# Performance work log

Hardware: AMD Instinct MI355X
Metric: run time of the kernel (lower is better)

## Reference

```python
import jax, jax.numpy as jnp
import numpy as np

D_MODEL = 1024
N_HEADS = 16
ADAPTIVE_TEMP = 1.0
LN_EPS = 1e-5


def _sinusoidal_pe(max_len, d_model):
    pos = np.arange(max_len)[:, None].astype(np.float32)
    div = np.exp(np.arange(0, d_model, 2).astype(np.float32) * (-np.log(10000.0) / d_model))
    pe = np.zeros((max_len, d_model), dtype=np.float32)
    pe[:, 0::2] = np.sin(pos * div)
    pe[:, 1::2] = np.cos(pos * div)
    return jnp.asarray(pe)


def _mlp2(q, w1, b1, w2, b2):
    # Linear(1,h) -> ReLU -> Linear(h,d)
    return jax.nn.relu(q @ w1 + b1) @ w2 + b2


def setup_inputs() -> dict:
    key = jax.random.key(0)
    ks = jax.random.split(key, 24)
    B, T, D = 2, 2048, D_MODEL
    H2 = D // 2
    s = 0.02
    inp = {
        "x": jax.random.normal(ks[0], (B, T, D), jnp.float32),
        "quantile": jax.random.uniform(ks[1], (B, 1), jnp.float32),
        "quantile_importance": jax.random.uniform(ks[2], (100,), jnp.float32),
        "Wq": jax.random.normal(ks[3], (D, D), jnp.float32) * s,
        "bq": jnp.zeros((D,), jnp.float32),
        "Wk": jax.random.normal(ks[4], (D, D), jnp.float32) * s,
        "bk": jnp.zeros((D,), jnp.float32),
        "Wv": jax.random.normal(ks[5], (D, D), jnp.float32) * s,
        "bv": jnp.zeros((D,), jnp.float32),
        "Wo": jax.random.normal(ks[6], (D, D), jnp.float32) * s,
        "bo": jnp.zeros((D,), jnp.float32),
        "qpq_w1": jax.random.normal(ks[7], (1, H2), jnp.float32) * s,
        "qpq_b1": jnp.zeros((H2,), jnp.float32),
        "qpq_w2": jax.random.normal(ks[8], (H2, D), jnp.float32) * s,
        "qpq_b2": jnp.zeros((D,), jnp.float32),
        "qpk_w1": jax.random.normal(ks[9], (1, H2), jnp.float32) * s,
        "qpk_b1": jnp.zeros((H2,), jnp.float32),
        "qpk_w2": jax.random.normal(ks[10], (H2, D), jnp.float32) * s,
        "qpk_b2": jnp.zeros((D,), jnp.float32),
        "qpv_w1": jax.random.normal(ks[11], (1, H2), jnp.float32) * s,
        "qpv_b1": jnp.zeros((H2,), jnp.float32),
        "qpv_w2": jax.random.normal(ks[12], (H2, D), jnp.float32) * s,
        "qpv_b2": jnp.zeros((D,), jnp.float32),
        "ln_g": jnp.ones((D,), jnp.float32),
        "ln_b": jnp.zeros((D,), jnp.float32),
    }
    return inp


def reference(x, quantile, quantile_importance,
              Wq, bq, Wk, bk, Wv, bv, Wo, bo,
              qpq_w1, qpq_b1, qpq_w2, qpq_b2,
              qpk_w1, qpk_b1, qpk_w2, qpk_b2,
              qpv_w1, qpv_b1, qpv_w2, qpv_b2,
              ln_g, ln_b):
    B, T, D = x.shape
    H = N_HEADS
    dk = D // H

    # positional encoding
    x = x + _sinusoidal_pe(T, D)

    # quantile-conditioned embeddings [B, D]
    q_embed = _mlp2(quantile, qpq_w1, qpq_b1, qpq_w2, qpq_b2)
    k_embed = _mlp2(quantile, qpk_w1, qpk_b1, qpk_w2, qpk_b2)
    v_embed = _mlp2(quantile, qpv_w1, qpv_b1, qpv_w2, qpv_b2)

    # importance weight per batch (no-grad buffer lookup)
    buf = jax.lax.stop_gradient(quantile_importance)
    idx = jnp.clip((quantile[:, 0] * 100).astype(jnp.int32), 0, 99)
    mx = buf.max()
    imp = buf[idx]
    imp = jnp.where(mx > 0, imp / mx, imp)  # [B]

    Q = (x @ Wq + bq) + q_embed[:, None, :]
    K = (x @ Wk + bk) + k_embed[:, None, :]
    V = (x @ Wv + bv) + v_embed[:, None, :]

    # [B, H, T, dk]
    Q = Q.reshape(B, T, H, dk).transpose(0, 2, 1, 3)
    K = K.reshape(B, T, H, dk).transpose(0, 2, 1, 3)
    V = V.reshape(B, T, H, dk).transpose(0, 2, 1, 3)

    scores = jnp.einsum('bhtd,bhsd->bhts', Q, K) / jnp.sqrt(jnp.float32(dk))
    scale = 1.0 + imp * ADAPTIVE_TEMP  # [B]
    scores = scores * scale[:, None, None, None]

    attn = jax.nn.softmax(scores, axis=-1)  # dropout is identity at inference
    out = jnp.einsum('bhts,bhsd->bhtd', attn, V)
    out = out.transpose(0, 2, 1, 3).reshape(B, T, D)
    out = out @ Wo + bo

    y = x + out
    mu = y.mean(axis=-1, keepdims=True)
    var = y.var(axis=-1, keepdims=True)
    return (y - mu) / jnp.sqrt(var + LN_EPS) * ln_g + ln_b
```

## Files before the change

kernel.cpp:

```cpp
#include <hip/hip_runtime.h>

#define D 1024
#define T 2048
#define BATCH 2
#define NR 4096
#define NH 16
#define HID 512

typedef unsigned short u16;
typedef unsigned int u32;
typedef unsigned long long u64;
typedef float f32x4 __attribute__((ext_vector_type(4)));
typedef float f32x16 __attribute__((ext_vector_type(16)));
typedef __bf16 bf16x8 __attribute__((ext_vector_type(8)));

__device__ __forceinline__ u16 f2bf(float f) {
    union { __bf16 h; u16 u; } c; c.h = (__bf16)f; return c.u;
}

__device__ __forceinline__ u32 cvtpk(float a, float b) {
    u32 r;
    asm("v_cvt_pk_bf16_f32 %0, %1, %2" : "=v"(r) : "v"(a), "v"(b));
    return r;
}

__device__ __forceinline__ void plswap(u32& x, u32& y) {
    asm volatile("v_permlane32_swap_b32 %0, %1" : "+v"(x), "+v"(y));
}

__device__ __forceinline__ float fmax3(float a, float b, float c) {
    float r; asm("v_max3_f32 %0, %1, %2, %3" : "=v"(r) : "v"(a), "v"(b), "v"(c)); return r;
}

__device__ __forceinline__ float vmax16(const f32x16& v) {
    float c0 = fmax3(v[0], v[1], v[2]);
    float c1 = fmax3(v[3], v[4], v[5]);
    float c2 = fmax3(v[6], v[7], v[8]);
    float c3 = fmax3(v[9], v[10], v[11]);
    c0 = fmax3(c0, v[12], v[13]);
    c1 = fmax3(c1, v[14], v[15]);
    c0 = fmax3(c0, c1, c2);
    return fmaxf(c0, c3);
}

__device__ __forceinline__ void gload16(const u16* g, u16* l) {
    __builtin_amdgcn_global_load_lds(
        (const __attribute__((address_space(1))) unsigned int*)g,
        (__attribute__((address_space(3))) unsigned int*)l,
        16, 0, 0);
}

__device__ __forceinline__ int swz8(int row) {
    return (row & 7) ^ ((row >> 3) & 3);
}

__global__ __launch_bounds__(256) void k_mlp1(const float* __restrict__ qtl,
        const float* __restrict__ w1q, const float* __restrict__ b1q, const float* __restrict__ w2q,
        const float* __restrict__ w1k, const float* __restrict__ b1k, const float* __restrict__ w2k,
        const float* __restrict__ w1v, const float* __restrict__ b1v, const float* __restrict__ w2v,
        const float* __restrict__ qimp, float* __restrict__ part, float* __restrict__ scl)
{
    int dc = blockIdx.x;
    int jc = blockIdx.y;
    int wb = blockIdx.z;
    int which = wb >> 1, b = wb & 1;
    const float *w1, *b1, *w2;
    if (which == 0)      { w1 = w1q; b1 = b1q; w2 = w2q; }
    else if (which == 1) { w1 = w1k; b1 = b1k; w2 = w2k; }
    else                 { w1 = w1v; b1 = b1v; w2 = w2v; }
    int tid = threadIdx.x;
    __shared__ float h[128];
    if (tid < 128) {
        int j = jc * 128 + tid;
        h[tid] = fmaxf(qtl[b] * w1[j] + b1[j], 0.0f);
    }
    __syncthreads();
    int d = dc * 256 + tid;
    float acc = 0.0f;
    for (int j = 0; j < 128; ++j) acc += h[j] * w2[(size_t)(jc * 128 + j) * D + d];
    part[((size_t)wb * 4 + jc) * D + d] = acc;
    if (dc == 0 && jc == 0 && wb == 0 && tid < BATCH) {
        float mx = qimp[0];
        for (int i = 1; i < 100; ++i) mx = fmaxf(mx, qimp[i]);
        float q = qtl[tid];
        int idx = (int)(q * 100.0f);
        idx = idx < 0 ? 0 : (idx > 99 ? 99 : idx);
        float imp = qimp[idx];
        if (mx > 0.0f) imp /= mx;
        scl[tid] = 1.0f + imp;
    }
}

__global__ __launch_bounds__(256) void k_mlp2(const float* __restrict__ part,
        const float* __restrict__ b2q, const float* __restrict__ b2k, const float* __restrict__ b2v,
        float* __restrict__ embeds)
{
    int dc = blockIdx.x;
    int wb = blockIdx.y;
    int which = wb >> 1;
    const float* b2 = which == 0 ? b2q : which == 1 ? b2k : b2v;
    int d = dc * 256 + threadIdx.x;
    float acc = b2[d];
    #pragma unroll
    for (int jc = 0; jc < 4; ++jc) acc += part[((size_t)wb * 4 + jc) * D + d];
    embeds[(size_t)wb * D + d] = acc;
}

__global__ __launch_bounds__(256) void k_pe(const float* __restrict__ x,
                                            float* __restrict__ xpe, u16* __restrict__ xpeb)
{
    int idx = (blockIdx.x * 256 + threadIdx.x) * 4;
    int d = idx & (D - 1);
    int t = (idx >> 10) & (T - 1);
    const float KL = -0.0089944731946f;
    float ft = (float)t;
    float dv0 = __expf((float)d * KL);
    float dv1 = __expf((float)(d + 2) * KL);
    float a0 = ft * dv0, a1 = ft * dv1;
    float4 xv = *reinterpret_cast<const float4*>(x + idx);
    float4 r;
    r.x = xv.x + __sinf(a0);
    r.y = xv.y + __cosf(a0);
    r.z = xv.z + __sinf(a1);
    r.w = xv.w + __cosf(a1);
    *reinterpret_cast<float4*>(xpe + idx) = r;
    ushort4 o;
    o.x = f2bf(r.x); o.y = f2bf(r.y); o.z = f2bf(r.z); o.w = f2bf(r.w);
    *reinterpret_cast<ushort4*>(xpeb + idx) = o;
}

__global__ __launch_bounds__(256) void k_wconv(const float* __restrict__ Wq, const float* __restrict__ Wk,
                                               const float* __restrict__ Wv, const float* __restrict__ Wo,
                                               u16* __restrict__ Wt)
{
    __shared__ float tile[64][65];
    int z = blockIdx.z;
    const float* W = z == 0 ? Wq : z == 1 ? Wk : z == 2 ? Wv : Wo;
    u16* out = Wt + (size_t)z * D * D;
    int n0 = blockIdx.x * 64, k0 = blockIdx.y * 64;
    int r = threadIdx.x >> 4;
    int c4 = (threadIdx.x & 15) * 4;
    #pragma unroll
    for (int rr = 0; rr < 64; rr += 16) {
        float4 v = *reinterpret_cast<const float4*>(W + (size_t)(k0 + r + rr) * D + n0 + c4);
        tile[r + rr][c4 + 0] = v.x; tile[r + rr][c4 + 1] = v.y;
        tile[r + rr][c4 + 2] = v.z; tile[r + rr][c4 + 3] = v.w;
    }
    __syncthreads();
    #pragma unroll
    for (int rr = 0; rr < 64; rr += 16) {
        ushort4 o;
        o.x = f2bf(tile[c4 + 0][r + rr]);
        o.y = f2bf(tile[c4 + 1][r + rr]);
        o.z = f2bf(tile[c4 + 2][r + rr]);
        o.w = f2bf(tile[c4 + 3][r + rr]);
        *reinterpret_cast<ushort4*>(out + (size_t)(n0 + r + rr) * D + k0 + c4) = o;
    }
}

__device__ __forceinline__ void gemm128(const u16* __restrict__ Ag, const u16* __restrict__ Bg,
                                        int m0, int n0, f32x4 acc[4][4])
{
    __shared__ u16 As[128 * 64];
    __shared__ u16 Bs[128 * 64];
    const int tid = threadIdx.x;
    const int lane = tid & 63, wave = tid >> 6;
    const int wr = wave >> 1, wc = wave & 1;
    #pragma unroll
    for (int i = 0; i < 4; ++i)
        #pragma unroll
        for (int j = 0; j < 4; ++j)
            #pragma unroll
            for (int e = 0; e < 4; ++e) acc[i][j][e] = 0.0f;

    for (int kt = 0; kt < 16; ++kt) {
        __syncthreads();
        #pragma unroll
        for (int c = 0; c < 4; ++c) {
            int ci = c * 256 + tid;
            int row = ci >> 3;
            int sl = (ci & 7) ^ (row & 7);
            gload16(Ag + (size_t)(m0 + row) * D + kt * 64 + sl * 8, As + (size_t)ci * 8);
            gload16(Bg + (size_t)(n0 + row) * D + kt * 64 + sl * 8, Bs + (size_t)ci * 8);
        }
        __syncthreads();
        #pragma unroll
        for (int ks = 0; ks < 2; ++ks) {
            bf16x8 af[4], bfr[4];
            #pragma unroll
            for (int i = 0; i < 4; ++i) {
                int ra = wr * 64 + i * 16 + (lane & 15);
                int sa = ((ks * 4 + (lane >> 4)) ^ (ra & 7));
                af[i] = *reinterpret_cast<const bf16x8*>((const char*)As + ra * 128 + sa * 16);
                int rb = wc * 64 + i * 16 + (lane & 15);
                int sb = ((ks * 4 + (lane >> 4)) ^ (rb & 7));
                bfr[i] = *reinterpret_cast<const bf16x8*>((const char*)Bs + rb * 128 + sb * 16);
            }
            #pragma unroll
            for (int i = 0; i < 4; ++i)
                #pragma unroll
                for (int j = 0; j < 4; ++j)
                    acc[i][j] = __builtin_amdgcn_mfma_f32_16x16x32_bf16(af[i], bfr[j], acc[i][j], 0, 0, 0);
        }
    }
}

__global__ __launch_bounds__(256, 2)
void k_qkv(const u16* __restrict__ A, const u16* __restrict__ Wt,
           const float* __restrict__ bq, const float* __restrict__ bk, const float* __restrict__ bv,
           const float* __restrict__ embeds, const float* __restrict__ scl,
           u16* __restrict__ Qo, u16* __restrict__ Ko, u16* __restrict__ Vt)
{
    int which = blockIdx.z;
    const u16* Bg = Wt + (size_t)which * D * D;
    const float* bias = which == 0 ? bq : which == 1 ? bk : bv;
    const float* emb = embeds + which * (BATCH * D);
    int m0 = blockIdx.x * 128, n0 = blockIdx.y * 128;
    f32x4 acc[4][4];
    gemm128(A, Bg, m0, n0, acc);
    int lane = threadIdx.x & 63, wave = threadIdx.x >> 6;
    int wr = wave >> 1, wc = wave & 1;
    int rowbase = m0 + wr * 64 + ((lane >> 4) << 2);
    int colbase = n0 + wc * 64 + (lane & 15);
    if (which < 2) {
        u16* Out = which == 0 ? Qo : Ko;
        float sc0 = 1.0f, sc1 = 1.0f;
        if (which == 0) {
            sc0 = scl[0] * 0.125f * 1.44269504f;
            sc1 = scl[1] * 0.125f * 1.44269504f;
        }
        #pragma unroll
        for (int j = 0; j < 4; ++j) {
            int c = colbase + j * 16;
            float add0 = bias[c] + emb[c];
            float add1 = bias[c] + emb[D + c];
            #pragma unroll
            for (int i = 0; i < 4; ++i) {
                int rb = rowbase + i * 16;
                #pragma unroll
                for (int jj = 0; jj < 4; ++jj) {
                    int r = rb + jj;
                    float v = (r >> 11) ? (acc[i][j][jj] + add1) * sc1
                                        : (acc[i][j][jj] + add0) * sc0;
                    Out[(size_t)r * D + c] = f2bf(v);
                }
            }
        }
    } else {
        #pragma unroll
        for (int j = 0; j < 4; ++j) {
            int c = colbase + j * 16;
            int hh = c >> 6, cc = c & 63;
            float add0 = bias[c] + emb[c];
            float add1 = bias[c] + emb[D + c];
            #pragma unroll
            for (int i = 0; i < 4; ++i) {
                int rb = rowbase + i * 16;
                int bb = rb >> 11;
                int t = rb & (T - 1);
                float add = bb ? add1 : add0;
                ushort4 o;
                o.x = f2bf(acc[i][j][0] + add);
                o.y = f2bf(acc[i][j][1] + add);
                o.z = f2bf(acc[i][j][2] + add);
                o.w = f2bf(acc[i][j][3] + add);
                *reinterpret_cast<ushort4*>(Vt + ((size_t)((bb * NH + hh) * 64 + cc)) * T + t) = o;
            }
        }
    }
}

__global__ __launch_bounds__(512, 4)
void k_attn(const u16* __restrict__ Q, const u16* __restrict__ K, const u16* __restrict__ Vt,
            u16* __restrict__ AO)
{
    __shared__ u16 Ks[2][2][64 * 64];
    __shared__ u16 Vs[2][2][64 * 64];
    int bh = blockIdx.x;
    int b = bh >> 4, hh = bh & 15;
    int q0 = blockIdx.y * 128;
    int tid = threadIdx.x;
    int lane = tid & 63, w = tid >> 6;
    int half = w >> 2, wq = w & 3;
    int q31 = lane & 31, h = lane >> 5;
    int sh = tid >> 8, sti = tid & 255;
    int kvb = sh * 1024;

    bf16x8 qf[4];
    {
        const u16* qp = Q + (size_t)(b * T + q0 + wq * 32 + q31) * D + hh * 64 + h * 8;
        #pragma unroll
        for (int ds = 0; ds < 4; ++ds)
            qf[ds] = *reinterpret_cast<const bf16x8*>(qp + ds * 16);
    }

    f32x16 o0, o1;
    #pragma unroll
    for (int e = 0; e < 16; ++e) { o0[e] = 0.0f; o1[e] = 0.0f; }
    float m_run = -1e30f, l_run = 0.0f;

    #pragma unroll
    for (int c = 0; c < 2; ++c) {
        int ci = c * 256 + sti;
        int row = ci >> 3;
        int sl = (ci & 7) ^ swz8(row);
        gload16(K + (size_t)(b * T + kvb + row) * D + hh * 64 + sl * 8, Ks[sh][0] + (size_t)ci * 8);
        gload16(Vt + (size_t)(bh * 64 + row) * T + kvb + sl * 8, Vs[sh][0] + (size_t)ci * 8);
    }
    __syncthreads();

    for (int kt = 0; kt < 16; ++kt) {
        int cur = kt & 1;
        if (kt < 15) {
            int t0 = kvb + (kt + 1) * 64;
            #pragma unroll
            for (int c = 0; c < 2; ++c) {
                int ci = c * 256 + sti;
                int row = ci >> 3;
                int sl = (ci & 7) ^ swz8(row);
                gload16(K + (size_t)(b * T + t0 + row) * D + hh * 64 + sl * 8, Ks[sh][cur ^ 1] + (size_t)ci * 8);
                gload16(Vt + (size_t)(bh * 64 + row) * T + t0 + sl * 8, Vs[sh][cur ^ 1] + (size_t)ci * 8);
            }
        }
        const char* Ksc = (const char*)Ks[half][cur];
        const char* Vsc = (const char*)Vs[half][cur];

        f32x16 s[2];
        #pragma unroll
        for (int k2 = 0; k2 < 2; ++k2)
            #pragma unroll
            for (int e = 0; e < 16; ++e) s[k2][e] = 0.0f;
        __builtin_amdgcn_s_setprio(1);
        #pragma unroll
        for (int k2 = 0; k2 < 2; ++k2) {
            int rk = k2 * 32 + q31;
            int xm = swz8(rk);
            #pragma unroll
            for (int ds = 0; ds < 4; ++ds) {
                int sp = (2 * ds + h) ^ xm;
                bf16x8 kf = *reinterpret_cast<const bf16x8*>(Ksc + rk * 128 + sp * 16);
                s[k2] = __builtin_amdgcn_mfma_f32_32x32x16_bf16(kf, qf[ds], s[k2], 0, 0, 0);
            }
        }
        __builtin_amdgcn_s_setprio(0);

        float mt = fmaxf(vmax16(s[0]), vmax16(s[1]));
        mt = fmaxf(mt, __shfl_xor(mt, 32, 64));
        bool skip = __all((int)(mt <= m_run + 11.0f));
        if (!skip) {
            float mn = fmaxf(m_run, mt);
            float corr = __builtin_exp2f(m_run - mn);
            m_run = mn;
            l_run *= corr;
            #pragma unroll
            for (int reg = 0; reg < 16; ++reg) {
                int src = ((reg & 3) + 8 * (reg >> 2)) + ((lane & 32) >> 3);
                float cr = __shfl(corr, src, 64);
                o0[reg] *= cr;
                o1[reg] *= cr;
            }
        }
        float ps0 = 0.0f, ps1 = 0.0f, ps2 = 0.0f, ps3 = 0.0f;
        #pragma unroll
        for (int k2 = 0; k2 < 2; ++k2)
            #pragma unroll
            for (int e = 0; e < 16; ++e) {
                float p = __builtin_exp2f(s[k2][e] - m_run);
                s[k2][e] = p;
                if ((e & 3) == 0) ps0 += p; else if ((e & 3) == 1) ps1 += p;
                else if ((e & 3) == 2) ps2 += p; else ps3 += p;
            }
        float psum = (ps0 + ps1) + (ps2 + ps3);
        psum += __shfl_xor(psum, 32, 64);
        l_run += psum;

        __builtin_amdgcn_s_setprio(1);
        #pragma unroll
        for (int k2 = 0; k2 < 2; ++k2) {
            u32 w0 = cvtpk(s[k2][0], s[k2][1]),   w1 = cvtpk(s[k2][2], s[k2][3]);
            u32 w2 = cvtpk(s[k2][4], s[k2][5]),   w3 = cvtpk(s[k2][6], s[k2][7]);
            u32 w4 = cvtpk(s[k2][8], s[k2][9]),   w5 = cvtpk(s[k2][10], s[k2][11]);
            u32 w6 = cvtpk(s[k2][12], s[k2][13]), w7 = cvtpk(s[k2][14], s[k2][15]);
            plswap(w0, w2); plswap(w1, w3);
            plswap(w4, w6); plswap(w5, w7);
            union { bf16x8 v; u32 u[4]; } plo, phi;
            plo.u[0] = w0; plo.u[1] = w1; plo.u[2] = w2; plo.u[3] = w3;
            phi.u[0] = w4; phi.u[1] = w5; phi.u[2] = w6; phi.u[3] = w7;
            int rv0 = q31, rv1 = 32 + q31;
            int x0 = swz8(rv0), x1 = swz8(rv1);
            int klo = 2 * k2, khi = 2 * k2 + 1;
            bf16x8 vf;
            vf = *reinterpret_cast<const bf16x8*>(Vsc + rv0 * 128 + (((2 * klo + h) ^ x0) << 4));
            o0 = __builtin_amdgcn_mfma_f32_32x32x16_bf16(plo.v, vf, o0, 0, 0, 0);
            vf = *reinterpret_cast<const bf16x8*>(Vsc + rv1 * 128 + (((2 * klo + h) ^ x1) << 4));
            o1 = __builtin_amdgcn_mfma_f32_32x32x16_bf16(plo.v, vf, o1, 0, 0, 0);
            vf = *reinterpret_cast<const bf16x8*>(Vsc + rv0 * 128 + (((2 * khi + h) ^ x0) << 4));
            o0 = __builtin_amdgcn_mfma_f32_32x32x16_bf16(phi.v, vf, o0, 0, 0, 0);
            vf = *reinterpret_cast<const bf16x8*>(Vsc + rv1 * 128 + (((2 * khi + h) ^ x1) << 4));
            o1 = __builtin_amdgcn_mfma_f32_32x32x16_bf16(phi.v, vf, o1, 0, 0, 0);
        }
        __builtin_amdgcn_s_setprio(0);
        __syncthreads();
    }

    float* ML = (float*)Ks;
    float* OB = (float*)Vs;
    if (half == 1) {
        if (h == 0) {
            ML[(wq * 2 + 0) * 32 + q31] = m_run;
            ML[(wq * 2 + 1) * 32 + q31] = l_run;
        }
        #pragma unroll
        for (int reg = 0; reg < 16; ++reg) {
            int row = (reg & 3) + 8 * (reg >> 2) + 4 * h;
            OB[((size_t)wq * 32 + row) * 64 + q31] = o0[reg];
            OB[((size_t)wq * 32 + row) * 64 + 32 + q31] = o1[reg];
        }
    }
    __syncthreads();
    if (half == 0) {
        float mB = ML[(wq * 2 + 0) * 32 + q31];
        float lB = ML[(wq * 2 + 1) * 32 + q31];
        float mn = fmaxf(m_run, mB);
        float ca = __builtin_exp2f(m_run - mn);
        float cb = __builtin_exp2f(mB - mn);
        float lf = ca * l_run + cb * lB;
        float fa = ca / lf, fb = cb / lf;
        #pragma unroll
        for (int reg = 0; reg < 16; ++reg) {
            int src = ((reg & 3) + 8 * (reg >> 2)) + ((lane & 32) >> 3);
            float far = __shfl(fa, src, 64);
            float fbr = __shfl(fb, src, 64);
            int row = (reg & 3) + 8 * (reg >> 2) + 4 * h;
            float b0 = OB[((size_t)wq * 32 + row) * 64 + q31];
            float b1 = OB[((size_t)wq * 32 + row) * 64 + 32 + q31];
            int qr = q0 + wq * 32 + row;
            size_t off = (size_t)(b * T + qr) * D + hh * 64 + q31;
            AO[off] = f2bf(o0[reg] * far + b0 * fbr);
            AO[off + 32] = f2bf(o1[reg] * far + b1 * fbr);
        }
    }
}

__global__ __launch_bounds__(256, 2)
void k_ogemm(const u16* __restrict__ A, const u16* __restrict__ Wt,
             const float* __restrict__ bo, const float* __restrict__ xpe,
             float* __restrict__ y)
{
    int m0 = blockIdx.x * 128, n0 = blockIdx.y * 128;
    f32x4 acc[4][4];
    gemm128(A, Wt, m0, n0, acc);
    int lane = threadIdx.x & 63, wave = threadIdx.x >> 6;
    int wr = wave >> 1, wc = wave & 1;
    int rowbase = m0 + wr * 64 + ((lane >> 4) << 2);
    int colbase = n0 + wc * 64 + (lane & 15);
    #pragma unroll
    for (int j = 0; j < 4; ++j) {
        int c = colbase + j * 16;
        float bc = bo[c];
        #pragma unroll
        for (int i = 0; i < 4; ++i) {
            #pragma unroll
            for (int jj = 0; jj < 4; ++jj) {
                int r = rowbase + i * 16 + jj;
                y[(size_t)r * D + c] = acc[i][j][jj] + bc + xpe[(size_t)r * D + c];
            }
        }
    }
}

__global__ __launch_bounds__(256) void k_ln(const float* __restrict__ y, const float* __restrict__ g,
                                            const float* __restrict__ bb, float* __restrict__ out)
{
    int row = blockIdx.x;
    int tid = threadIdx.x;
    const float* yr = y + (size_t)row * D;
    float4 v = *reinterpret_cast<const float4*>(yr + tid * 4);
    float s = v.x + v.y + v.z + v.w;
    float s2 = v.x * v.x + v.y * v.y + v.z * v.z + v.w * v.w;
    #pragma unroll
    for (int off = 1; off < 64; off <<= 1) {
        s += __shfl_xor(s, off, 64);
        s2 += __shfl_xor(s2, off, 64);
    }
    __shared__ float red[8];
    int wave = tid >> 6, lane = tid & 63;
    if (lane == 0) { red[wave] = s; red[4 + wave] = s2; }
    __syncthreads();
    s = red[0] + red[1] + red[2] + red[3];
    s2 = red[4] + red[5] + red[6] + red[7];
    float mu = s * (1.0f / 1024.0f);
    float var = s2 * (1.0f / 1024.0f) - mu * mu;
    float rstd = rsqrtf(var + 1e-5f);
    float4 gv = *reinterpret_cast<const float4*>(g + tid * 4);
    float4 bv = *reinterpret_cast<const float4*>(bb + tid * 4);
    float4 o;
    o.x = (v.x - mu) * rstd * gv.x + bv.x;
    o.y = (v.y - mu) * rstd * gv.y + bv.y;
    o.z = (v.z - mu) * rstd * gv.z + bv.z;
    o.w = (v.w - mu) * rstd * gv.w + bv.w;
    *reinterpret_cast<float4*>(out + (size_t)row * D + tid * 4) = o;
}

extern "C" void kernel_launch(void* const* d_in, const int* in_sizes, int n_in,
                              void* d_out, int out_size, void* d_ws, size_t ws_size,
                              hipStream_t stream)
{
    const float* x    = (const float*)d_in[0];
    const float* qtl  = (const float*)d_in[1];
    const float* qimp = (const float*)d_in[2];
    const float* Wq = (const float*)d_in[3];
    const float* bq = (const float*)d_in[4];
    const float* Wk = (const float*)d_in[5];
    const float* bk = (const float*)d_in[6];
    const float* Wv = (const float*)d_in[7];
    const float* bv = (const float*)d_in[8];
    const float* Wo = (const float*)d_in[9];
    const float* bo = (const float*)d_in[10];
    const float* qpq_w1 = (const float*)d_in[11];
    const float* qpq_b1 = (const float*)d_in[12];
    const float* qpq_w2 = (const float*)d_in[13];
    const float* qpq_b2 = (const float*)d_in[14];
    const float* qpk_w1 = (const float*)d_in[15];
    const float* qpk_b1 = (const float*)d_in[16];
    const float* qpk_w2 = (const float*)d_in[17];
    const float* qpk_b2 = (const float*)d_in[18];
    const float* qpv_w1 = (const float*)d_in[19];
    const float* qpv_b1 = (const float*)d_in[20];
    const float* qpv_w2 = (const float*)d_in[21];
    const float* qpv_b2 = (const float*)d_in[22];
    const float* ln_g = (const float*)d_in[23];
    const float* ln_b = (const float*)d_in[24];
    (void)in_sizes; (void)n_in; (void)out_size; (void)ws_size;

    char* w = (char*)d_ws;
    float* xpe   = (float*)(w);
    u16* xpeb    = (u16*)(w + (16u << 20));
    u16* Wt      = (u16*)(w + (24u << 20));
    u16* Qb      = (u16*)(w + (32u << 20));
    u16* Kb      = (u16*)(w + (40u << 20));
    u16* Vtb     = (u16*)(w + (48u << 20));
    u16* AOb     = (u16*)(w + (56u << 20));
    float* yb    = (float*)(w + (32u << 20));
    float* emb   = (float*)(w + (64u << 20));
    float* scl   = (float*)(w + (64u << 20) + 32768);
    float* part  = (float*)(w + (64u << 20) + 65536);

    k_mlp1<<<dim3(4, 4, 6), 256, 0, stream>>>(qtl,
        qpq_w1, qpq_b1, qpq_w2,
        qpk_w1, qpk_b1, qpk_w2,
        qpv_w1, qpv_b1, qpv_w2,
        qimp, part, scl);
    k_mlp2<<<dim3(4, 6), 256, 0, stream>>>(part, qpq_b2, qpk_b2, qpv_b2, emb);
    k_pe<<<4096, 256, 0, stream>>>(x, xpe, xpeb);
    k_wconv<<<dim3(16, 16, 4), 256, 0, stream>>>(Wq, Wk, Wv, Wo, Wt);
    k_qkv<<<dim3(32, 8, 3), 256, 0, stream>>>(xpeb, Wt, bq, bk, bv, emb, scl, Qb, Kb, Vtb);
    k_attn<<<dim3(32, 16), 512, 0, stream>>>(Qb, Kb, Vtb, AOb);
    k_ogemm<<<dim3(32, 8), 256, 0, stream>>>(AOb, Wt + (size_t)3 * D * D, bo, xpe, yb);
    k_ln<<<4096, 256, 0, stream>>>(yb, ln_g, ln_b, (float*)d_out);
}
```

Baseline: 159.9 us.

## Load K/V fragments directly from global memory instead of staging in LDS

Removes the double-buffered LDS staging of K and V tiles (global_load_lds plus swizzle) in the attention kernel. Each lane now reads its K and V MFMA fragments straight from global memory, relying on L2/L1 caching, which also removes the per-iteration __syncthreads. This trades LDS traffic and barriers for repeated global loads: the four query waves of a half now each fetch the same K/V data separately, and the loads are no longer software-prefetched one tile ahead.

```diff
diff --git a/kernel.cpp b/kernel.cpp
--- a/kernel.cpp
+++ b/kernel.cpp
@@ -48,10 +48,6 @@
         (const __attribute__((address_space(1))) unsigned int*)g,
         (__attribute__((address_space(3))) unsigned int*)l,
         16, 0, 0);
-}
-
-__device__ __forceinline__ int swz8(int row) {
-    return (row & 7) ^ ((row >> 3) & 3);
 }
 
 __global__ __launch_bounds__(256) void k_mlp1(const float* __restrict__ qtl,
@@ -274,8 +270,8 @@
 void k_attn(const u16* __restrict__ Q, const u16* __restrict__ K, const u16* __restrict__ Vt,
             u16* __restrict__ AO)
 {
-    __shared__ u16 Ks[2][2][64 * 64];
-    __shared__ u16 Vs[2][2][64 * 64];
+    __shared__ float ML[4 * 2 * 32];
+    __shared__ float OB[4 * 32 * 64];
     int bh = blockIdx.x;
     int b = bh >> 4, hh = bh & 15;
     int q0 = blockIdx.y * 128;
@@ -283,8 +279,7 @@
     int lane = tid & 63, w = tid >> 6;
     int half = w >> 2, wq = w & 3;
     int q31 = lane & 31, h = lane >> 5;
-    int sh = tid >> 8, sti = tid & 255;
-    int kvb = sh * 1024;
+    int kvb = half * 1024;
 
     bf16x8 qf[4];
     {
@@ -294,37 +289,17 @@
             qf[ds] = *reinterpret_cast<const bf16x8*>(qp + ds * 16);
     }
 
+    const u16* kp0 = K + (size_t)(b * T + kvb + q31) * D + hh * 64;
+    const u16* kp1 = kp0 + (size_t)32 * D;
+    const u16* vp0 = Vt + (size_t)(bh * 64 + q31) * T + kvb;
+    const u16* vp1 = vp0 + (size_t)32 * T;
+
     f32x16 o0, o1;
     #pragma unroll
     for (int e = 0; e < 16; ++e) { o0[e] = 0.0f; o1[e] = 0.0f; }
     float m_run = -1e30f, l_run = 0.0f;
 
-    #pragma unroll
-    for (int c = 0; c < 2; ++c) {
-        int ci = c * 256 + sti;
-        int row = ci >> 3;
-        int sl = (ci & 7) ^ swz8(row);
-        gload16(K + (size_t)(b * T + kvb + row) * D + hh * 64 + sl * 8, Ks[sh][0] + (size_t)ci * 8);
-        gload16(Vt + (size_t)(bh * 64 + row) * T + kvb + sl * 8, Vs[sh][0] + (size_t)ci * 8);
-    }
-    __syncthreads();
-
     for (int kt = 0; kt < 16; ++kt) {
-        int cur = kt & 1;
-        if (kt < 15) {
-            int t0 = kvb + (kt + 1) * 64;
-            #pragma unroll
-            for (int c = 0; c < 2; ++c) {
-                int ci = c * 256 + sti;
-                int row = ci >> 3;
-                int sl = (ci & 7) ^ swz8(row);
-                gload16(K + (size_t)(b * T + t0 + row) * D + hh * 64 + sl * 8, Ks[sh][cur ^ 1] + (size_t)ci * 8);
-                gload16(Vt + (size_t)(bh * 64 + row) * T + t0 + sl * 8, Vs[sh][cur ^ 1] + (size_t)ci * 8);
-            }
-        }
-        const char* Ksc = (const char*)Ks[half][cur];
-        const char* Vsc = (const char*)Vs[half][cur];
-
         f32x16 s[2];
         #pragma unroll
         for (int k2 = 0; k2 < 2; ++k2)
@@ -332,15 +307,11 @@
             for (int e = 0; e < 16; ++e) s[k2][e] = 0.0f;
         __builtin_amdgcn_s_setprio(1);
         #pragma unroll
-        for (int k2 = 0; k2 < 2; ++k2) {
-            int rk = k2 * 32 + q31;
-            int xm = swz8(rk);
-            #pragma unroll
-            for (int ds = 0; ds < 4; ++ds) {
-                int sp = (2 * ds + h) ^ xm;
-                bf16x8 kf = *reinterpret_cast<const bf16x8*>(Ksc + rk * 128 + sp * 16);
-                s[k2] = __builtin_amdgcn_mfma_f32_32x32x16_bf16(kf, qf[ds], s[k2], 0, 0, 0);
-            }
+        for (int ds = 0; ds < 4; ++ds) {
+            bf16x8 kf0 = *reinterpret_cast<const bf16x8*>(kp0 + ds * 16 + h * 8);
+            bf16x8 kf1 = *reinterpret_cast<const bf16x8*>(kp1 + ds * 16 + h * 8);
+            s[0] = __builtin_amdgcn_mfma_f32_32x32x16_bf16(kf0, qf[ds], s[0], 0, 0, 0);
+            s[1] = __builtin_amdgcn_mfma_f32_32x32x16_bf16(kf1, qf[ds], s[1], 0, 0, 0);
         }
         __builtin_amdgcn_s_setprio(0);
 
@@ -386,25 +357,22 @@
             union { bf16x8 v; u32 u[4]; } plo, phi;
             plo.u[0] = w0; plo.u[1] = w1; plo.u[2] = w2; plo.u[3] = w3;
             phi.u[0] = w4; phi.u[1] = w5; phi.u[2] = w6; phi.u[3] = w7;
-            int rv0 = q31, rv1 = 32 + q31;
-            int x0 = swz8(rv0), x1 = swz8(rv1);
             int klo = 2 * k2, khi = 2 * k2 + 1;
             bf16x8 vf;
-            vf = *reinterpret_cast<const bf16x8*>(Vsc + rv0 * 128 + (((2 * klo + h) ^ x0) << 4));
+            vf = *reinterpret_cast<const bf16x8*>(vp0 + klo * 16 + h * 8);
             o0 = __builtin_amdgcn_mfma_f32_32x32x16_bf16(plo.v, vf, o0, 0, 0, 0);
-            vf = *reinterpret_cast<const bf16x8*>(Vsc + rv1 * 128 + (((2 * klo + h) ^ x1) << 4));
+            vf = *reinterpret_cast<const bf16x8*>(vp1 + klo * 16 + h * 8);
             o1 = __builtin_amdgcn_mfma_f32_32x32x16_bf16(plo.v, vf, o1, 0, 0, 0);
-            vf = *reinterpret_cast<const bf16x8*>(Vsc + rv0 * 128 + (((2 * khi + h) ^ x0) << 4));
+            vf = *reinterpret_cast<const bf16x8*>(vp0 + khi * 16 + h * 8);
             o0 = __builtin_amdgcn_mfma_f32_32x32x16_bf16(phi.v, vf, o0, 0, 0, 0);
-            vf = *reinterpret_cast<const bf16x8*>(Vsc + rv1 * 128 + (((2 * khi + h) ^ x1) << 4));
+            vf = *reinterpret_cast<const bf16x8*>(vp1 + khi * 16 + h * 8);
             o1 = __builtin_amdgcn_mfma_f32_32x32x16_bf16(phi.v, vf, o1, 0, 0, 0);
         }
         __builtin_amdgcn_s_setprio(0);
-        __syncthreads();
-    }
-
-    float* ML = (float*)Ks;
-    float* OB = (float*)Vs;
+        kp0 += (size_t)64 * D;  kp1 += (size_t)64 * D;
+        vp0 += 64;              vp1 += 64;
+    }
+
     if (half == 1) {
         if (h == 0) {
             ML[(wq * 2 + 0) * 32 + q31] = m_run;
```

After: 219.7 us. 37.4% more time.

## Double-buffer GEMM LDS tiles and merge PE and weight-convert kernels

Applied to the files above, without the earlier changes.

The shared bf16 GEMM helper now uses two LDS buffers for A and B. The next K-tile's global-to-LDS loads are issued before the MFMAs on the current tile, and each iteration needs only one barrier instead of two. Separately, the positional-encoding add and the weight transpose/convert kernels are merged into one launch that dispatches on block index, saving a launch and letting the two overlap. Doubling LDS per block to 64 KB may reduce the occupancy target of two blocks per CU in the QKV and output GEMMs. The prefetch also relies on gload16 completing before the end-of-iteration barrier.

```diff
diff --git a/kernel.cpp b/kernel.cpp
--- a/kernel.cpp
+++ b/kernel.cpp
@@ -106,38 +106,39 @@
     embeds[(size_t)wb * D + d] = acc;
 }
 
-__global__ __launch_bounds__(256) void k_pe(const float* __restrict__ x,
-                                            float* __restrict__ xpe, u16* __restrict__ xpeb)
-{
-    int idx = (blockIdx.x * 256 + threadIdx.x) * 4;
-    int d = idx & (D - 1);
-    int t = (idx >> 10) & (T - 1);
-    const float KL = -0.0089944731946f;
-    float ft = (float)t;
-    float dv0 = __expf((float)d * KL);
-    float dv1 = __expf((float)(d + 2) * KL);
-    float a0 = ft * dv0, a1 = ft * dv1;
-    float4 xv = *reinterpret_cast<const float4*>(x + idx);
-    float4 r;
-    r.x = xv.x + __sinf(a0);
-    r.y = xv.y + __cosf(a0);
-    r.z = xv.z + __sinf(a1);
-    r.w = xv.w + __cosf(a1);
-    *reinterpret_cast<float4*>(xpe + idx) = r;
-    ushort4 o;
-    o.x = f2bf(r.x); o.y = f2bf(r.y); o.z = f2bf(r.z); o.w = f2bf(r.w);
-    *reinterpret_cast<ushort4*>(xpeb + idx) = o;
-}
-
-__global__ __launch_bounds__(256) void k_wconv(const float* __restrict__ Wq, const float* __restrict__ Wk,
-                                               const float* __restrict__ Wv, const float* __restrict__ Wo,
-                                               u16* __restrict__ Wt)
-{
+__global__ __launch_bounds__(256) void k_prep(const float* __restrict__ x,
+                                              float* __restrict__ xpe, u16* __restrict__ xpeb,
+                                              const float* __restrict__ Wq, const float* __restrict__ Wk,
+                                              const float* __restrict__ Wv, const float* __restrict__ Wo,
+                                              u16* __restrict__ Wt)
+{
+    if (blockIdx.x < 4096) {
+        int idx = (blockIdx.x * 256 + threadIdx.x) * 4;
+        int d = idx & (D - 1);
+        int t = (idx >> 10) & (T - 1);
+        const float KL = -0.0089944731946f;
+        float ft = (float)t;
+        float dv0 = __expf((float)d * KL);
+        float dv1 = __expf((float)(d + 2) * KL);
+        float a0 = ft * dv0, a1 = ft * dv1;
+        float4 xv = *reinterpret_cast<const float4*>(x + idx);
+        float4 r;
+        r.x = xv.x + __sinf(a0);
+        r.y = xv.y + __cosf(a0);
+        r.z = xv.z + __sinf(a1);
+        r.w = xv.w + __cosf(a1);
+        *reinterpret_cast<float4*>(xpe + idx) = r;
+        ushort4 o;
+        o.x = f2bf(r.x); o.y = f2bf(r.y); o.z = f2bf(r.z); o.w = f2bf(r.w);
+        *reinterpret_cast<ushort4*>(xpeb + idx) = o;
+        return;
+    }
     __shared__ float tile[64][65];
-    int z = blockIdx.z;
+    int bi = blockIdx.x - 4096;
+    int z = bi >> 8;
     const float* W = z == 0 ? Wq : z == 1 ? Wk : z == 2 ? Wv : Wo;
     u16* out = Wt + (size_t)z * D * D;
-    int n0 = blockIdx.x * 64, k0 = blockIdx.y * 64;
+    int n0 = (bi & 15) * 64, k0 = ((bi >> 4) & 15) * 64;
     int r = threadIdx.x >> 4;
     int c4 = (threadIdx.x & 15) * 4;
     #pragma unroll
@@ -161,8 +162,8 @@
 __device__ __forceinline__ void gemm128(const u16* __restrict__ Ag, const u16* __restrict__ Bg,
                                         int m0, int n0, f32x4 acc[4][4])
 {
-    __shared__ u16 As[128 * 64];
-    __shared__ u16 Bs[128 * 64];
+    __shared__ u16 As[2][128 * 64];
+    __shared__ u16 Bs[2][128 * 64];
     const int tid = threadIdx.x;
     const int lane = tid & 63, wave = tid >> 6;
     const int wr = wave >> 1, wc = wave & 1;
@@ -173,17 +174,29 @@
             #pragma unroll
             for (int e = 0; e < 4; ++e) acc[i][j][e] = 0.0f;
 
+    #pragma unroll
+    for (int c = 0; c < 4; ++c) {
+        int ci = c * 256 + tid;
+        int row = ci >> 3;
+        int sl = (ci & 7) ^ (row & 7);
+        gload16(Ag + (size_t)(m0 + row) * D + sl * 8, As[0] + (size_t)ci * 8);
+        gload16(Bg + (size_t)(n0 + row) * D + sl * 8, Bs[0] + (size_t)ci * 8);
+    }
+    __syncthreads();
+
     for (int kt = 0; kt < 16; ++kt) {
-        __syncthreads();
-        #pragma unroll
-        for (int c = 0; c < 4; ++c) {
-            int ci = c * 256 + tid;
-            int row = ci >> 3;
-            int sl = (ci & 7) ^ (row & 7);
-            gload16(Ag + (size_t)(m0 + row) * D + kt * 64 + sl * 8, As + (size_t)ci * 8);
-            gload16(Bg + (size_t)(n0 + row) * D + kt * 64 + sl * 8, Bs + (size_t)ci * 8);
-        }
-        __syncthreads();
+        int cur = kt & 1;
+        if (kt < 15) {
+            int k0 = (kt + 1) * 64;
+            #pragma unroll
+            for (int c = 0; c < 4; ++c) {
+                int ci = c * 256 + tid;
+                int row = ci >> 3;
+                int sl = (ci & 7) ^ (row & 7);
+                gload16(Ag + (size_t)(m0 + row) * D + k0 + sl * 8, As[cur ^ 1] + (size_t)ci * 8);
+                gload16(Bg + (size_t)(n0 + row) * D + k0 + sl * 8, Bs[cur ^ 1] + (size_t)ci * 8);
+            }
+        }
         #pragma unroll
         for (int ks = 0; ks < 2; ++ks) {
             bf16x8 af[4], bfr[4];
@@ -191,10 +204,10 @@
             for (int i = 0; i < 4; ++i) {
                 int ra = wr * 64 + i * 16 + (lane & 15);
                 int sa = ((ks * 4 + (lane >> 4)) ^ (ra & 7));
-                af[i] = *reinterpret_cast<const bf16x8*>((const char*)As + ra * 128 + sa * 16);
+                af[i] = *reinterpret_cast<const bf16x8*>((const char*)As[cur] + ra * 128 + sa * 16);
                 int rb = wc * 64 + i * 16 + (lane & 15);
                 int sb = ((ks * 4 + (lane >> 4)) ^ (rb & 7));
-                bfr[i] = *reinterpret_cast<const bf16x8*>((const char*)Bs + rb * 128 + sb * 16);
+                bfr[i] = *reinterpret_cast<const bf16x8*>((const char*)Bs[cur] + rb * 128 + sb * 16);
             }
             #pragma unroll
             for (int i = 0; i < 4; ++i)
@@ -202,6 +215,7 @@
                 for (int j = 0; j < 4; ++j)
                     acc[i][j] = __builtin_amdgcn_mfma_f32_16x16x32_bf16(af[i], bfr[j], acc[i][j], 0, 0, 0);
         }
+        __syncthreads();
     }
 }
 
@@ -552,8 +566,7 @@
         qpv_w1, qpv_b1, qpv_w2,
         qimp, part, scl);
     k_mlp2<<<dim3(4, 6), 256, 0, stream>>>(part, qpq_b2, qpk_b2, qpv_b2, emb);
-    k_pe<<<4096, 256, 0, stream>>>(x, xpe, xpeb);
-    k_wconv<<<dim3(16, 16, 4), 256, 0, stream>>>(Wq, Wk, Wv, Wo, Wt);
+    k_prep<<<5120, 256, 0, stream>>>(x, xpe, xpeb, Wq, Wk, Wv, Wo, Wt);
     k_qkv<<<dim3(32, 8, 3), 256, 0, stream>>>(xpeb, Wt, bq, bk, bv, emb, scl, Qb, Kb, Vtb);
     k_attn<<<dim3(32, 16), 512, 0, stream>>>(Qb, Kb, Vtb, AOb);
     k_ogemm<<<dim3(32, 8), 256, 0, stream>>>(AOb, Wt + (size_t)3 * D * D, bo, xpe, yb);
```

Result: slower. 167.0 us (+4.4%).
